# Kernel tuning notes

Hardware: AMD Instinct MI355X
Metric: run time of the kernel (lower is better)

## Reference

```python
import jax, jax.numpy as jnp
import numpy as np

B, S, HID = 2, 2048, 2048
NH, NKV = 16, 4
HD = HID // NH  # 128
GROUPS = NH // NKV


def _rope(x, cos, sin):
    # x: [B, S, H, D]; cos/sin: [S, D//2]
    xr = x.reshape(*x.shape[:-1], HD // 2, 2)
    x0, x1 = xr[..., 0], xr[..., 1]
    c = cos[None, :, None, :]
    s = sin[None, :, None, :]
    o0 = x0 * c - x1 * s
    o1 = x0 * s + x1 * c
    return jnp.stack([o0, o1], axis=-1).reshape(*x.shape)


def setup_inputs() -> dict:
    key = jax.random.key(0)
    k1, k2, k3, k4, k5, k6 = jax.random.split(key, 6)
    hidden_states = jax.random.normal(k1, (B, S, HID), dtype=jnp.float32)
    # RoPE frequencies (llama-style)
    inv_freq = 1.0 / (10000.0 ** (np.arange(0, HD, 2, dtype=np.float32) / HD))
    t = np.arange(S, dtype=np.float32)
    ang = np.outer(t, inv_freq)  # [S, HD//2]
    freqs_cos = jnp.asarray(np.cos(ang), dtype=jnp.float32)
    freqs_sin = jnp.asarray(np.sin(ang), dtype=jnp.float32)
    # additive causal mask [1,1,S,S]
    causal = jnp.triu(jnp.full((S, S), -1e9, dtype=jnp.float32), k=1)
    attention_mask = causal[None, None]
    sc = 0.02
    Wq = jax.random.normal(k2, (NH * HD, HID), dtype=jnp.float32) * sc
    Wk = jax.random.normal(k3, (NKV * HD, HID), dtype=jnp.float32) * sc
    Wv = jax.random.normal(k4, (NKV * HD, HID), dtype=jnp.float32) * sc
    Wo = jax.random.normal(k5, (HID, NH * HD), dtype=jnp.float32) * sc
    return {"hidden_states": hidden_states, "freqs_cos": freqs_cos,
            "freqs_sin": freqs_sin, "attention_mask": attention_mask,
            "Wq": Wq, "Wk": Wk, "Wv": Wv, "Wo": Wo}


def reference(hidden_states, freqs_cos, freqs_sin, attention_mask, Wq, Wk, Wv, Wo):
    xq = (hidden_states @ Wq.T).reshape(B, S, NH, HD)
    xk = (hidden_states @ Wk.T).reshape(B, S, NKV, HD)
    xv = (hidden_states @ Wv.T).reshape(B, S, NKV, HD)
    xq = _rope(xq, freqs_cos, freqs_sin)
    xk = _rope(xk, freqs_cos, freqs_sin)
    # expand KV heads for GQA: [B,S,NKV,D] -> [B,S,NH,D]
    xk = jnp.repeat(xk, GROUPS, axis=2)
    xv = jnp.repeat(xv, GROUPS, axis=2)
    q = xq.transpose(0, 2, 1, 3)  # [B,H,S,D]
    k = xk.transpose(0, 2, 1, 3)
    v = xv.transpose(0, 2, 1, 3)
    scores = jnp.einsum('bhqd,bhkd->bhqk', q, k) / jnp.sqrt(jnp.float32(HD))
    scores = scores + attention_mask
    probs = jax.nn.softmax(scores, axis=-1)
    out = jnp.einsum('bhqk,bhkd->bhqd', probs, v)
    out = out.transpose(0, 2, 1, 3).reshape(B, S, NH * HD)
    return out @ Wo.T
```

## Files before the change

### kernel.cpp

```cpp
#include <hip/hip_runtime.h>


typedef __attribute__((ext_vector_type(8))) short bf16x8;
typedef __attribute__((ext_vector_type(4))) float f32x4;
typedef unsigned short u16;

#define B_   2
#define S_   2048
#define HID_ 2048
#define NH_  16
#define NKV_ 4
#define HD_  128

__device__ __forceinline__ u16 f2bf(float f) {
  unsigned u = __float_as_uint(f);
  u = (u + 0x7FFFu + ((u >> 16) & 1u)) >> 16;
  return (u16)u;
}
__device__ __forceinline__ float bf2f(u16 h) {
  return __uint_as_float(((unsigned)h) << 16);
}

__device__ __forceinline__ void gl_lds16(const void* g, void* l) {
  __builtin_amdgcn_global_load_lds(
      (const __attribute__((address_space(1))) void*)g,
      (__attribute__((address_space(3))) void*)l, 16, 0, 0);
}

__global__ void convert_bf16(const float* __restrict__ src, u16* __restrict__ dst, int n8) {
  int i = blockIdx.x * 256 + threadIdx.x;
  if (i >= n8) return;
  const float4* s = (const float4*)src + (size_t)i * 2;
  float4 a = s[0], b = s[1];
  union { u16 u[8]; uint4 v; } o;
  o.u[0] = f2bf(a.x); o.u[1] = f2bf(a.y); o.u[2] = f2bf(a.z); o.u[3] = f2bf(a.w);
  o.u[4] = f2bf(b.x); o.u[5] = f2bf(b.y); o.u[6] = f2bf(b.z); o.u[7] = f2bf(b.w);
  ((uint4*)dst)[i] = o.v;
}

template<int EPI>
__launch_bounds__(256, 2)
__global__ void gemm128(const u16* __restrict__ A, const u16* __restrict__ Bm,
                        float* __restrict__ C, u16* __restrict__ Qb,
                        u16* __restrict__ Kb, u16* __restrict__ Vb,
                        int N, int K)
{
  __shared__ u16 As[128 * 64];
  __shared__ u16 Bs[128 * 64];
  const int tid = threadIdx.x;
  const int lane = tid & 63;
  const int w = tid >> 6;
  const int lo = lane & 15, hi = lane >> 4;
  const int wr = w >> 1, wc = w & 1;
  const int rowA0 = blockIdx.x * 128;
  const int rowB0 = blockIdx.y * 128;

  f32x4 acc[4][4] = {};

  for (int kt = 0; kt < K; kt += 64) {
    __syncthreads();
#pragma unroll
    for (int it = 0; it < 4; ++it) {
      int c = it * 256 + tid;
      int r = c >> 3;
      int cb = (c & 7) * 8;
      gl_lds16(A + (size_t)(rowA0 + r) * K + kt + cb, (char*)As + c * 16);
      gl_lds16(Bm + (size_t)(rowB0 + r) * K + kt + cb, (char*)Bs + c * 16);
    }
    __syncthreads();
#pragma unroll
    for (int kk = 0; kk < 64; kk += 32) {
      bf16x8 af[4], bfr[4];
#pragma unroll
      for (int m = 0; m < 4; ++m)
        af[m] = *(const bf16x8*)(As + (wr * 64 + m * 16 + lo) * 64 + kk + hi * 8);
#pragma unroll
      for (int n = 0; n < 4; ++n)
        bfr[n] = *(const bf16x8*)(Bs + (wc * 64 + n * 16 + lo) * 64 + kk + hi * 8);
#pragma unroll
      for (int m = 0; m < 4; ++m)
#pragma unroll
        for (int n = 0; n < 4; ++n)
          acc[m][n] = __builtin_amdgcn_mfma_f32_16x16x32_bf16(af[m], bfr[n], acc[m][n], 0, 0, 0);
    }
  }

#pragma unroll
  for (int m = 0; m < 4; ++m) {
#pragma unroll
    for (int n = 0; n < 4; ++n) {
#pragma unroll
      for (int r = 0; r < 4; ++r) {
        int grow = rowA0 + wr * 64 + m * 16 + hi * 4 + r;
        int gcol = rowB0 + wc * 64 + n * 16 + lo;
        float v = acc[m][n][r];
        if (EPI == 0) {
          C[(size_t)grow * N + gcol] = v;
        } else {
          int bb = grow >> 11, s = grow & 2047;
          u16 hv = f2bf(v);
          if (gcol < 2048) {
            int h = gcol >> 7, d = gcol & 127;
            Qb[(((size_t)bb * NH_ + h) * S_ + s) * HD_ + d] = hv;
          } else if (gcol < 2560) {
            int h = (gcol - 2048) >> 7, d = gcol & 127;
            Kb[(((size_t)bb * NKV_ + h) * S_ + s) * HD_ + d] = hv;
          } else {
            int h = (gcol - 2560) >> 7, d = gcol & 127;
            Vb[(((size_t)bb * NKV_ + h) * S_ + s) * HD_ + d] = hv;
          }
        }
      }
    }
  }
}

__global__ void rope_k(u16* __restrict__ Qb, u16* __restrict__ Kb,
                       const float* __restrict__ fcos, const float* __restrict__ fsin)
{
  int idx = blockIdx.x * 256 + threadIdx.x;
  int chunk = idx & 15;
  int s = (idx >> 4) & 2047;
  int hs = idx >> 15;
  u16* p = (hs < 32) ? (Qb + ((size_t)hs * S_ + s) * HD_ + chunk * 8)
                     : (Kb + ((size_t)(hs - 32) * S_ + s) * HD_ + chunk * 8);
  uint4 raw = *(uint4*)p;
  float4 c4 = *(const float4*)(fcos + (size_t)s * 64 + chunk * 4);
  float4 s4 = *(const float4*)(fsin + (size_t)s * 64 + chunk * 4);
  float cc[4] = {c4.x, c4.y, c4.z, c4.w};
  float ss[4] = {s4.x, s4.y, s4.z, s4.w};
  unsigned* rw = (unsigned*)&raw;
#pragma unroll
  for (int j = 0; j < 4; ++j) {
    float x0 = bf2f((u16)(rw[j] & 0xFFFFu));
    float x1 = bf2f((u16)(rw[j] >> 16));
    float o0 = x0 * cc[j] - x1 * ss[j];
    float o1 = x0 * ss[j] + x1 * cc[j];
    rw[j] = (unsigned)f2bf(o0) | ((unsigned)f2bf(o1) << 16);
  }
  *(uint4*)p = raw;
}

__global__ void transpose_v(const u16* __restrict__ Vb, u16* __restrict__ Vtg)
{
  __shared__ u16 t[64][65];
  const int st = blockIdx.x, dt = blockIdx.y, hs = blockIdx.z;
  const u16* src = Vb + ((size_t)hs * S_ + st * 64) * HD_ + dt * 64;
#pragma unroll
  for (int it = 0; it < 2; ++it) {
    int c = it * 256 + threadIdx.x;
    int r = c >> 3, cb = (c & 7) * 8;
    uint4 v = *(const uint4*)(src + (size_t)r * HD_ + cb);
    u16* u = (u16*)&v;
#pragma unroll
    for (int e = 0; e < 8; ++e) t[r][cb + e] = u[e];
  }
  __syncthreads();
#pragma unroll
  for (int it = 0; it < 2; ++it) {
    int c = it * 256 + threadIdx.x;
    int r2 = c >> 3, cb2 = (c & 7) * 8;
    union { u16 u[8]; uint4 v; } o;
#pragma unroll
    for (int e = 0; e < 8; ++e) o.u[e] = t[cb2 + e][r2];
    *(uint4*)(Vtg + ((size_t)hs * HD_ + dt * 64 + r2) * S_ + st * 64 + cb2) = o.v;
  }
}

__launch_bounds__(256, 2)
__global__ void flash_attn(const u16* __restrict__ Qb, const u16* __restrict__ Kb,
                           const u16* __restrict__ Vtg, u16* __restrict__ AO)
{
  __shared__ u16 Ks[2][64 * 128];
  __shared__ u16 Vt[2][128 * 64];
  __shared__ u16 Ps[4][16 * 72];

  const int tid = threadIdx.x, lane = tid & 63, w = tid >> 6;
  const int lo = lane & 15, hi = lane >> 4;
  const int h = blockIdx.y, b = blockIdx.z;
  const int kvh = h >> 2;
  const u16* Qh = Qb + (((size_t)b * NH_ + h) * S_) * HD_;
  const u16* Kh = Kb + (((size_t)b * NKV_ + kvh) * S_) * HD_;
  const u16* Vh = Vtg + (((size_t)b * NKV_ + kvh) * HD_) * S_;

  auto STAGE = [&](int buf, int kt) {
#pragma unroll
    for (int it = 0; it < 4; ++it) {
      int c = it * 256 + tid;
      int r = c >> 4;
      int slot = (c & 15) ^ (r & 7);
      gl_lds16(Kh + (size_t)(kt + r) * HD_ + slot * 8, (char*)Ks[buf] + c * 16);
    }
#pragma unroll
    for (int it = 0; it < 4; ++it) {
      int c = it * 256 + tid;
      int r = c >> 3;
      int slot = (c & 7) ^ (r & 7);
      gl_lds16(Vh + (size_t)r * S_ + kt + slot * 8, (char*)Vt[buf] + c * 16);
    }
  };

  const float scale = 0.08838834764831845f;

  for (int pass = 0; pass < 2; ++pass) {
    const int qblk = pass ? (31 - (int)blockIdx.x) : (int)blockIdx.x;
    const int qbase = qblk * 64;

    bf16x8 qf[4];
    const int qrow = qbase + w * 16 + lo;
#pragma unroll
    for (int kk = 0; kk < 4; ++kk)
      qf[kk] = *(const bf16x8*)(Qh + (size_t)qrow * HD_ + kk * 32 + hi * 8);

    f32x4 o[8] = {};
    float mrow[4], lrow[4];
#pragma unroll
    for (int r = 0; r < 4; ++r) { mrow[r] = -3e38f; lrow[r] = 0.f; }

    __syncthreads();
    STAGE(0, 0);
    asm volatile("s_waitcnt vmcnt(0)" ::: "memory");
    __syncthreads();
    int cur = 0;

    for (int t = 0; t <= qblk; ++t) {
      if (t < qblk) STAGE(cur ^ 1, (t + 1) * 64);
      const int kt = t * 64;

      f32x4 sc[4] = {};
      __builtin_amdgcn_s_setprio(1);
#pragma unroll
      for (int kk = 0; kk < 4; ++kk) {
        bf16x8 kf[4];
#pragma unroll
        for (int n = 0; n < 4; ++n) {
          int row = n * 16 + lo;
          int slot = (kk * 4 + hi) ^ (row & 7);
          kf[n] = *(const bf16x8*)((const char*)Ks[cur] + row * 256 + slot * 16);
        }
#pragma unroll
        for (int n = 0; n < 4; ++n)
          sc[n] = __builtin_amdgcn_mfma_f32_16x16x32_bf16(qf[kk], kf[n], sc[n], 0, 0, 0);
      }
      __builtin_amdgcn_s_setprio(0);

      float p[4][4];
      float tmax[4];
#pragma unroll
      for (int r = 0; r < 4; ++r) tmax[r] = -3e38f;
      const bool diag = (t == qblk);
#pragma unroll
      for (int n = 0; n < 4; ++n) {
        int kv = kt + n * 16 + lo;
#pragma unroll
        for (int r = 0; r < 4; ++r) {
          float v = sc[n][r] * scale;
          if (diag && kv > qbase + w * 16 + hi * 4 + r) v = -1e9f;
          p[n][r] = v;
          tmax[r] = fmaxf(tmax[r], v);
        }
      }
#pragma unroll
      for (int d = 1; d < 16; d <<= 1)
#pragma unroll
        for (int r = 0; r < 4; ++r)
          tmax[r] = fmaxf(tmax[r], __shfl_xor(tmax[r], d));
      float resc[4], lsum[4];
#pragma unroll
      for (int r = 0; r < 4; ++r) {
        float mn = fmaxf(mrow[r], tmax[r]);
        resc[r] = __expf(mrow[r] - mn);
        mrow[r] = mn;
        lsum[r] = 0.f;
      }
#pragma unroll
      for (int n = 0; n < 4; ++n)
#pragma unroll
        for (int r = 0; r < 4; ++r) {
          float pv = __expf(p[n][r] - mrow[r]);
          p[n][r] = pv;
          lsum[r] += pv;
        }
#pragma unroll
      for (int d = 1; d < 16; d <<= 1)
#pragma unroll
        for (int r = 0; r < 4; ++r)
          lsum[r] += __shfl_xor(lsum[r], d);
#pragma unroll
      for (int r = 0; r < 4; ++r)
        lrow[r] = lrow[r] * resc[r] + lsum[r];
#pragma unroll
      for (int nf = 0; nf < 8; ++nf)
#pragma unroll
        for (int r = 0; r < 4; ++r)
          o[nf][r] *= resc[r];

#pragma unroll
      for (int n = 0; n < 4; ++n)
#pragma unroll
        for (int r = 0; r < 4; ++r)
          Ps[w][(hi * 4 + r) * 72 + n * 16 + lo] = f2bf(p[n][r]);

      __builtin_amdgcn_s_setprio(1);
#pragma unroll
      for (int kk2 = 0; kk2 < 64; kk2 += 32) {
        bf16x8 pa = *(const bf16x8*)(&Ps[w][lo * 72 + kk2 + hi * 8]);
#pragma unroll
        for (int nf = 0; nf < 8; ++nf) {
          int row = nf * 16 + lo;
          int slot = ((kk2 >> 3) + hi) ^ (row & 7);
          bf16x8 vf = *(const bf16x8*)((const char*)Vt[cur] + row * 128 + slot * 16);
          o[nf] = __builtin_amdgcn_mfma_f32_16x16x32_bf16(pa, vf, o[nf], 0, 0, 0);
        }
      }
      __builtin_amdgcn_s_setprio(0);

      asm volatile("s_waitcnt vmcnt(0)" ::: "memory");
      __syncthreads();
      cur ^= 1;
    }

#pragma unroll
    for (int r = 0; r < 4; ++r) {
      float inv = 1.f / lrow[r];
      int srow = qbase + w * 16 + hi * 4 + r;
      size_t base = ((size_t)b * S_ + srow) * HID_ + (size_t)h * HD_;
#pragma unroll
      for (int nf = 0; nf < 8; ++nf)
        AO[base + nf * 16 + lo] = f2bf(o[nf][r] * inv);
    }
  }
}

extern "C" void kernel_launch(void* const* d_in, const int* in_sizes, int n_in,
                              void* d_out, int out_size, void* d_ws, size_t ws_size,
                              hipStream_t stream)
{
  (void)in_sizes; (void)n_in; (void)out_size; (void)ws_size;
  const float* X  = (const float*)d_in[0];
  const float* fc = (const float*)d_in[1];
  const float* fs = (const float*)d_in[2];
  const float* Wq = (const float*)d_in[4];
  const float* Wk = (const float*)d_in[5];
  const float* Wv = (const float*)d_in[6];
  const float* Wo = (const float*)d_in[7];
  float* out = (float*)d_out;

  u16* Xb  = (u16*)d_ws;
  u16* Wb  = Xb + (size_t)4096 * 2048;
  u16* Qb  = Wb + (size_t)3072 * 2048;
  u16* Kb  = Qb + (size_t)B_ * NH_ * S_ * HD_;
  u16* Vb  = Kb + (size_t)B_ * NKV_ * S_ * HD_;
  u16* AO  = Xb;
  u16* Wob = Wb;
  u16* Vtg = Wb + (size_t)2048 * 2048;

  convert_bf16<<<4096, 256, 0, stream>>>(X,  Xb,               4096 * 2048 / 8);
  convert_bf16<<<2048, 256, 0, stream>>>(Wq, Wb,               2048 * 2048 / 8);
  convert_bf16<<<512,  256, 0, stream>>>(Wk, Wb + 2048 * 2048, 512 * 2048 / 8);
  convert_bf16<<<512,  256, 0, stream>>>(Wv, Wb + 2560 * 2048, 512 * 2048 / 8);

  gemm128<1><<<dim3(32, 24), 256, 0, stream>>>(Xb, Wb, nullptr, Qb, Kb, Vb, 3072, 2048);

  convert_bf16<<<2048, 256, 0, stream>>>(Wo, Wob, 2048 * 2048 / 8);

  transpose_v<<<dim3(32, 2, 8), 256, 0, stream>>>(Vb, Vtg);

  rope_k<<<5120, 256, 0, stream>>>(Qb, Kb, fc, fs);

  flash_attn<<<dim3(16, NH_, B_), 256, 0, stream>>>(Qb, Kb, Vtg, AO);

  gemm128<0><<<dim3(32, 16), 256, 0, stream>>>(AO, Wob, out, nullptr, nullptr, nullptr, 2048, 2048);
}
```

Before: 232.8 us.

## Rewrite flash attention with 32x32 MFMA, register-resident P, 256-row query blocks

Flash attention now uses 8 waves per block, each owning 32 query rows, and computes S^T = K·Q^T with 32x32x16 bf16 MFMAs so each lane holds one query row's scores. The row max and sum need only in-register reductions plus one cross-half shuffle. P is packed to bf16 with v_cvt_pk and exchanged between lane halves through shuffles instead of an LDS round trip. Softmax uses exp2 with a folded scale, and waves skip KV tiles that are fully masked. Query blocks grow to 256 rows, which cuts the grid to 128 blocks of 512 threads and may lower occupancy and worsen load balance on the causal diagonal.

```diff
diff --git a/kernel.cpp b/kernel.cpp
--- a/kernel.cpp
+++ b/kernel.cpp
@@ -3,6 +3,8 @@
 
 typedef __attribute__((ext_vector_type(8))) short bf16x8;
 typedef __attribute__((ext_vector_type(4))) float f32x4;
+typedef __attribute__((ext_vector_type(16))) float f32x16;
+typedef __attribute__((ext_vector_type(4))) unsigned short u16x4;
 typedef unsigned short u16;
 
 #define B_   2
@@ -167,168 +169,170 @@
   }
 }
 
-__launch_bounds__(256, 2)
+__launch_bounds__(512, 2)
 __global__ void flash_attn(const u16* __restrict__ Qb, const u16* __restrict__ Kb,
                            const u16* __restrict__ Vtg, u16* __restrict__ AO)
 {
   __shared__ u16 Ks[2][64 * 128];
   __shared__ u16 Vt[2][128 * 64];
-  __shared__ u16 Ps[4][16 * 72];
 
   const int tid = threadIdx.x, lane = tid & 63, w = tid >> 6;
-  const int lo = lane & 15, hi = lane >> 4;
-  const int h = blockIdx.y, b = blockIdx.z;
-  const int kvh = h >> 2;
-  const u16* Qh = Qb + (((size_t)b * NH_ + h) * S_) * HD_;
-  const u16* Kh = Kb + (((size_t)b * NKV_ + kvh) * S_) * HD_;
-  const u16* Vh = Vtg + (((size_t)b * NKV_ + kvh) * HD_) * S_;
-
-  auto STAGE = [&](int buf, int kt) {
-#pragma unroll
-    for (int it = 0; it < 4; ++it) {
-      int c = it * 256 + tid;
-      int r = c >> 4;
-      int slot = (c & 15) ^ (r & 7);
-      gl_lds16(Kh + (size_t)(kt + r) * HD_ + slot * 8, (char*)Ks[buf] + c * 16);
-    }
-#pragma unroll
-    for (int it = 0; it < 4; ++it) {
-      int c = it * 256 + tid;
-      int r = c >> 3;
-      int slot = (c & 7) ^ (r & 7);
-      gl_lds16(Vh + (size_t)r * S_ + kt + slot * 8, (char*)Vt[buf] + c * 16);
-    }
-  };
-
-  const float scale = 0.08838834764831845f;
+  const int ql = lane & 31, hh = lane >> 5;
+  const int h = blockIdx.y, b = blockIdx.z, kvh = h >> 2;
+  const u16* Qh = Qb + ((size_t)b * NH_ + h) * S_ * HD_;
+  const u16* Kh = Kb + ((size_t)b * NKV_ + kvh) * S_ * HD_;
+  const u16* Vh = Vtg + ((size_t)b * NKV_ + kvh) * HD_ * S_;
+  const float cf = 0.12752704581383682f;
+  const float NEG = -30000.f;
 
   for (int pass = 0; pass < 2; ++pass) {
-    const int qblk = pass ? (31 - (int)blockIdx.x) : (int)blockIdx.x;
-    const int qbase = qblk * 64;
-
-    bf16x8 qf[4];
-    const int qrow = qbase + w * 16 + lo;
-#pragma unroll
-    for (int kk = 0; kk < 4; ++kk)
-      qf[kk] = *(const bf16x8*)(Qh + (size_t)qrow * HD_ + kk * 32 + hi * 8);
-
-    f32x4 o[8] = {};
-    float mrow[4], lrow[4];
-#pragma unroll
-    for (int r = 0; r < 4; ++r) { mrow[r] = -3e38f; lrow[r] = 0.f; }
+    const int qb = pass ? (7 - (int)blockIdx.x) : (int)blockIdx.x;
+    const int q0w = qb * 256 + w * 32;
+    const int qg = q0w + ql;
+    const int nt = qb * 4 + 4;
+
+    bf16x8 qf[8];
+#pragma unroll
+    for (int s = 0; s < 8; ++s)
+      qf[s] = *(const bf16x8*)(Qh + (size_t)qg * HD_ + s * 16 + hh * 8);
+
+    f32x16 o[4] = {};
+    float m = NEG, l = 0.f;
 
     __syncthreads();
-    STAGE(0, 0);
-    asm volatile("s_waitcnt vmcnt(0)" ::: "memory");
+#pragma unroll
+    for (int it = 0; it < 2; ++it) {
+      int ck = it * 512 + tid; int r = ck >> 4; int slot = (ck & 15) ^ (r & 7);
+      gl_lds16(Kh + (size_t)r * HD_ + slot * 8, (char*)Ks[0] + ck * 16);
+    }
+#pragma unroll
+    for (int it = 0; it < 2; ++it) {
+      int cv = it * 512 + tid; int r = cv >> 3; int slot = (cv & 7) ^ (r & 7);
+      gl_lds16(Vh + (size_t)r * S_ + slot * 8, (char*)Vt[0] + cv * 16);
+    }
     __syncthreads();
     int cur = 0;
 
-    for (int t = 0; t <= qblk; ++t) {
-      if (t < qblk) STAGE(cur ^ 1, (t + 1) * 64);
+    for (int t = 0; t < nt; ++t) {
+      if (t < nt - 1) {
+        const int kn = (t + 1) * 64;
+#pragma unroll
+        for (int it = 0; it < 2; ++it) {
+          int ck = it * 512 + tid; int r = ck >> 4; int slot = (ck & 15) ^ (r & 7);
+          gl_lds16(Kh + (size_t)(kn + r) * HD_ + slot * 8, (char*)Ks[cur ^ 1] + ck * 16);
+        }
+#pragma unroll
+        for (int it = 0; it < 2; ++it) {
+          int cv = it * 512 + tid; int r = cv >> 3; int slot = (cv & 7) ^ (r & 7);
+          gl_lds16(Vh + (size_t)r * S_ + kn + slot * 8, (char*)Vt[cur ^ 1] + cv * 16);
+        }
+      }
       const int kt = t * 64;
-
-      f32x4 sc[4] = {};
-      __builtin_amdgcn_s_setprio(1);
-#pragma unroll
-      for (int kk = 0; kk < 4; ++kk) {
-        bf16x8 kf[4];
-#pragma unroll
-        for (int n = 0; n < 4; ++n) {
-          int row = n * 16 + lo;
-          int slot = (kk * 4 + hi) ^ (row & 7);
-          kf[n] = *(const bf16x8*)((const char*)Ks[cur] + row * 256 + slot * 16);
-        }
-#pragma unroll
-        for (int n = 0; n < 4; ++n)
-          sc[n] = __builtin_amdgcn_mfma_f32_16x16x32_bf16(qf[kk], kf[n], sc[n], 0, 0, 0);
+      if (kt < q0w + 32) {
+        f32x16 st[2] = {};
+        __builtin_amdgcn_s_setprio(1);
+#pragma unroll
+        for (int sl = 0; sl < 8; ++sl) {
+          int slot = ((2 * sl + hh) ^ (ql & 7)) * 16;
+          bf16x8 k0 = *(const bf16x8*)((const char*)Ks[cur] + ql * 256 + slot);
+          bf16x8 k1 = *(const bf16x8*)((const char*)Ks[cur] + (32 + ql) * 256 + slot);
+          st[0] = __builtin_amdgcn_mfma_f32_32x32x16_bf16(k0, qf[sl], st[0], 0, 0, 0);
+          st[1] = __builtin_amdgcn_mfma_f32_32x32x16_bf16(k1, qf[sl], st[1], 0, 0, 0);
+        }
+        __builtin_amdgcn_s_setprio(0);
+
+        if ((kt + 63) > q0w) {
+#pragma unroll
+          for (int i = 0; i < 2; ++i)
+#pragma unroll
+            for (int r = 0; r < 16; ++r) {
+              int kv = kt + 32 * i + (r & 3) + 8 * (r >> 2) + 4 * hh;
+              if (kv > qg) st[i][r] = NEG;
+            }
+        }
+
+        float mx[8];
+#pragma unroll
+        for (int r = 0; r < 8; ++r)
+          mx[r] = fmaxf(fmaxf(st[0][r], st[0][r + 8]), fmaxf(st[1][r], st[1][r + 8]));
+#pragma unroll
+        for (int d = 4; d > 0; d >>= 1)
+#pragma unroll
+          for (int r = 0; r < d; ++r) mx[r] = fmaxf(mx[r], mx[r + d]);
+        float tmax = fmaxf(mx[0], __shfl_xor(mx[0], 32));
+
+        float mn = fmaxf(m, tmax);
+        float rs = __builtin_exp2f((m - mn) * cf);
+        m = mn; l *= rs;
+#pragma unroll
+        for (int dt = 0; dt < 4; ++dt)
+#pragma unroll
+          for (int r = 0; r < 16; ++r) o[dt][r] *= rs;
+
+        const float mc = m * cf;
+#pragma unroll
+        for (int i = 0; i < 2; ++i)
+#pragma unroll
+          for (int r = 0; r < 16; ++r)
+            st[i][r] = __builtin_exp2f(__builtin_fmaf(st[i][r], cf, -mc));
+        float sm[8];
+#pragma unroll
+        for (int r = 0; r < 8; ++r)
+          sm[r] = (st[0][r] + st[0][r + 8]) + (st[1][r] + st[1][r + 8]);
+#pragma unroll
+        for (int d = 4; d > 0; d >>= 1)
+#pragma unroll
+          for (int r = 0; r < d; ++r) sm[r] += sm[r + d];
+        l += sm[0] + __shfl_xor(sm[0], 32);
+
+        bf16x8 pb[4];
+#pragma unroll
+        for (int i = 0; i < 2; ++i)
+#pragma unroll
+          for (int s = 0; s < 2; ++s) {
+            unsigned wA, wC, wB, wD;
+            asm("v_cvt_pk_bf16_f32 %0, %1, %2" : "=v"(wA) : "v"(st[i][8*s+0]), "v"(st[i][8*s+1]));
+            asm("v_cvt_pk_bf16_f32 %0, %1, %2" : "=v"(wC) : "v"(st[i][8*s+2]), "v"(st[i][8*s+3]));
+            asm("v_cvt_pk_bf16_f32 %0, %1, %2" : "=v"(wB) : "v"(st[i][8*s+4]), "v"(st[i][8*s+5]));
+            asm("v_cvt_pk_bf16_f32 %0, %1, %2" : "=v"(wD) : "v"(st[i][8*s+6]), "v"(st[i][8*s+7]));
+            unsigned tA = (unsigned)__shfl_xor((int)wA, 32);
+            unsigned tB = (unsigned)__shfl_xor((int)wB, 32);
+            unsigned tC = (unsigned)__shfl_xor((int)wC, 32);
+            unsigned tD = (unsigned)__shfl_xor((int)wD, 32);
+            union { unsigned u[4]; bf16x8 v; } pk;
+            pk.u[0] = hh ? tB : wA;
+            pk.u[1] = hh ? tD : wC;
+            pk.u[2] = hh ? wB : tA;
+            pk.u[3] = hh ? wD : tC;
+            pb[2 * i + s] = pk.v;
+          }
+
+        __builtin_amdgcn_s_setprio(1);
+#pragma unroll
+        for (int dt = 0; dt < 4; ++dt)
+#pragma unroll
+          for (int ks = 0; ks < 4; ++ks) {
+            int row = 32 * dt + ql;
+            bf16x8 vf = *(const bf16x8*)((const char*)Vt[cur] + row * 128 +
+                                         (((2 * ks + hh) ^ (ql & 7)) * 16));
+            o[dt] = __builtin_amdgcn_mfma_f32_32x32x16_bf16(vf, pb[ks], o[dt], 0, 0, 0);
+          }
+        __builtin_amdgcn_s_setprio(0);
       }
-      __builtin_amdgcn_s_setprio(0);
-
-      float p[4][4];
-      float tmax[4];
-#pragma unroll
-      for (int r = 0; r < 4; ++r) tmax[r] = -3e38f;
-      const bool diag = (t == qblk);
-#pragma unroll
-      for (int n = 0; n < 4; ++n) {
-        int kv = kt + n * 16 + lo;
-#pragma unroll
-        for (int r = 0; r < 4; ++r) {
-          float v = sc[n][r] * scale;
-          if (diag && kv > qbase + w * 16 + hi * 4 + r) v = -1e9f;
-          p[n][r] = v;
-          tmax[r] = fmaxf(tmax[r], v);
-        }
-      }
-#pragma unroll
-      for (int d = 1; d < 16; d <<= 1)
-#pragma unroll
-        for (int r = 0; r < 4; ++r)
-          tmax[r] = fmaxf(tmax[r], __shfl_xor(tmax[r], d));
-      float resc[4], lsum[4];
-#pragma unroll
-      for (int r = 0; r < 4; ++r) {
-        float mn = fmaxf(mrow[r], tmax[r]);
-        resc[r] = __expf(mrow[r] - mn);
-        mrow[r] = mn;
-        lsum[r] = 0.f;
-      }
-#pragma unroll
-      for (int n = 0; n < 4; ++n)
-#pragma unroll
-        for (int r = 0; r < 4; ++r) {
-          float pv = __expf(p[n][r] - mrow[r]);
-          p[n][r] = pv;
-          lsum[r] += pv;
-        }
-#pragma unroll
-      for (int d = 1; d < 16; d <<= 1)
-#pragma unroll
-        for (int r = 0; r < 4; ++r)
-          lsum[r] += __shfl_xor(lsum[r], d);
-#pragma unroll
-      for (int r = 0; r < 4; ++r)
-        lrow[r] = lrow[r] * resc[r] + lsum[r];
-#pragma unroll
-      for (int nf = 0; nf < 8; ++nf)
-#pragma unroll
-        for (int r = 0; r < 4; ++r)
-          o[nf][r] *= resc[r];
-
-#pragma unroll
-      for (int n = 0; n < 4; ++n)
-#pragma unroll
-        for (int r = 0; r < 4; ++r)
-          Ps[w][(hi * 4 + r) * 72 + n * 16 + lo] = f2bf(p[n][r]);
-
-      __builtin_amdgcn_s_setprio(1);
-#pragma unroll
-      for (int kk2 = 0; kk2 < 64; kk2 += 32) {
-        bf16x8 pa = *(const bf16x8*)(&Ps[w][lo * 72 + kk2 + hi * 8]);
-#pragma unroll
-        for (int nf = 0; nf < 8; ++nf) {
-          int row = nf * 16 + lo;
-          int slot = ((kk2 >> 3) + hi) ^ (row & 7);
-          bf16x8 vf = *(const bf16x8*)((const char*)Vt[cur] + row * 128 + slot * 16);
-          o[nf] = __builtin_amdgcn_mfma_f32_16x16x32_bf16(pa, vf, o[nf], 0, 0, 0);
-        }
-      }
-      __builtin_amdgcn_s_setprio(0);
-
-      asm volatile("s_waitcnt vmcnt(0)" ::: "memory");
       __syncthreads();
       cur ^= 1;
     }
 
-#pragma unroll
-    for (int r = 0; r < 4; ++r) {
-      float inv = 1.f / lrow[r];
-      int srow = qbase + w * 16 + hi * 4 + r;
-      size_t base = ((size_t)b * S_ + srow) * HID_ + (size_t)h * HD_;
-#pragma unroll
-      for (int nf = 0; nf < 8; ++nf)
-        AO[base + nf * 16 + lo] = f2bf(o[nf][r] * inv);
-    }
+    const float inv = 1.f / l;
+#pragma unroll
+    for (int dt = 0; dt < 4; ++dt)
+#pragma unroll
+      for (int g = 0; g < 4; ++g) {
+        u16x4 pk4;
+#pragma unroll
+        for (int e = 0; e < 4; ++e) pk4[e] = f2bf(o[dt][4 * g + e] * inv);
+        *(u16x4*)(AO + ((size_t)b * S_ + qg) * HID_ + h * HD_ + 32 * dt + 8 * g + 4 * hh) = pk4;
+      }
   }
 }
 
@@ -368,7 +372,7 @@
 
   rope_k<<<5120, 256, 0, stream>>>(Qb, Kb, fc, fs);
 
-  flash_attn<<<dim3(16, NH_, B_), 256, 0, stream>>>(Qb, Kb, Vtg, AO);
+  flash_attn<<<dim3(4, NH_, B_), 512, 0, stream>>>(Qb, Kb, Vtg, AO);
 
   gemm128<0><<<dim3(32, 16), 256, 0, stream>>>(AO, Wob, out, nullptr, nullptr, nullptr, 2048, 2048);
 }
```

Measured after the change: 266.0 us. 14.3% more time.
